# Kernel optimization log

Measured on AMD Instinct MI355X. Metric: run time of the kernel, lower is better.

## Reference

```python
import jax, jax.numpy as jnp
import numpy as np

N_RAYS = 32768
HID = 64
MARCH_ITERS = 64
EPS = 1e-4
NEAR = 0.0
FAR = 1.0
T_FAR = 1.0
TPUT_B = 64
JITTER = 1.0 / TPUT_B  # fixed stand-in for random.random() * (2 / batch_size)


def _init_linear(key, fan_in, fan_out):
    kw, kb = jax.random.split(key)
    lim = 1.0 / np.sqrt(fan_in)
    W = jax.random.uniform(kw, (fan_in, fan_out), jnp.float32, -lim, lim)
    b = jax.random.uniform(kb, (fan_out,), jnp.float32, -lim, lim)
    return W, b


def setup_inputs() -> dict:
    key = jax.random.key(0)
    ks = jax.random.split(key, 6)
    rays = jax.random.normal(ks[0], (N_RAYS, 6), jnp.float32)
    W0, b0 = _init_linear(ks[1], 3, HID)
    W1, b1 = _init_linear(ks[2], HID, HID)
    W2, b2 = _init_linear(ks[3], HID, 1)
    Wr0, br0 = _init_linear(ks[4], 6, HID)
    Wr1, br1 = _init_linear(ks[5], HID, 3)
    return dict(rays=rays, W0=W0, b0=b0, W1=W1, b1=b1, W2=W2, b2=b2,
                Wr0=Wr0, br0=br0, Wr1=Wr1, br1=br1)


def _sdf(p, W0, b0, W1, b1, W2, b2):
    # p: [N, 3] -> signed distance [N, 1]
    h = jax.nn.relu(p @ W0 + b0)
    h = jax.nn.relu(h @ W1 + b1)
    return h @ W2 + b2


def _refl(p, d, Wr0, br0, Wr1, br1):
    # p, d: [N, 3] -> RGB [N, 3]
    h = jax.nn.relu(jnp.concatenate([p, d], axis=-1) @ Wr0 + br0)
    return jax.nn.sigmoid(h @ Wr1 + br1)


def reference(rays, W0, b0, W1, b1, W2, b2, Wr0, br0, Wr1, br1):
    r_o, r_d = rays[..., :3], rays[..., 3:]
    sdf = lambda p: _sdf(p, W0, b0, W1, b1, W2, b2)

    # --- sphere march (64 fixed iterations; early-exit break is a no-op
    # once all rays hit, since hit rays stop updating) ---
    hits0 = jnp.zeros(r_o.shape[:-1] + (1,), jnp.bool_)
    dist0 = jnp.full(r_o.shape[:-1] + (1,), NEAR, jnp.float32)

    def march(carry, _):
        hits, cd = carry
        d = sdf(r_o + r_d * cd)  # [N, 1]
        hits = hits | ((d < EPS) & (cd >= NEAR) & (cd <= FAR))
        cd = jnp.where(~hits, cd + d, cd)
        return (hits, cd), None

    (hit, t), _ = jax.lax.scan(march, (hits0, dist0), None, length=MARCH_ITERS)
    pts = r_o + r_d * t

    rgb = _refl(pts, r_d, Wr0, br0, Wr1, br1)
    rgb = jnp.where(hit, rgb, 0.0)  # out[~hit] = 0

    # --- throughput (index search under no_grad in the original) ---
    max_t = T_FAR + JITTER
    step = max_t / TPUT_B
    sg = jax.lax.stop_gradient
    sdf_ng = lambda p: _sdf(p, sg(W0), sg(b0), sg(W1), sg(b1), sg(W2), sg(b2))
    r_o_ng, r_d_ng = sg(r_o), sg(r_d)

    curr_min0 = sdf_ng(r_o_ng)[..., 0]          # [N]
    idxs0 = jnp.zeros_like(curr_min0, jnp.int32)

    def tloop(carry, i):
        cm, idxs = carry
        t_i = step * (i + 1).astype(jnp.float32)
        sd = sdf_ng(r_o_ng + t_i * r_d_ng)[..., 0]
        idxs = jnp.where(sd < cm, i + 1, idxs)
        return (jnp.minimum(cm, sd), idxs), None

    (_, idxs), _ = jax.lax.scan(tloop, (curr_min0, idxs0),
                                jnp.arange(TPUT_B, dtype=jnp.int32))

    best_pos = r_o + idxs[..., None].astype(jnp.float32) * step * r_d  # [N, 3]
    tput = sdf(best_pos)  # [N, 1], differentiable (outside no_grad in torch)

    return jnp.concatenate([rgb, tput], axis=-1)  # [N, 4]
```

## Files before the change

kernel.cpp:

```cpp
#include <hip/hip_runtime.h>
#include <math.h>

#define NRAYS        32768
#define MARCH_ITERS  64
#define EPS_         1e-4f
#define STEP_        ((1.0f + 1.0f/64.0f) / 64.0f)

typedef __attribute__((ext_vector_type(8)))  short    short8;
typedef __attribute__((ext_vector_type(4)))  float    float4v;
typedef __attribute__((ext_vector_type(2)))  float    float2v;
typedef __attribute__((ext_vector_type(4)))  unsigned uint4v;

__device__ __forceinline__ short8 mk_frag(unsigned p0, unsigned p1,
                                          unsigned p2, unsigned p3) {
    uint4v v = {p0, p1, p2, p3};
    return __builtin_bit_cast(short8, v);
}

__device__ __forceinline__ unsigned packbf(unsigned a, unsigned b) {
    return __builtin_amdgcn_perm(b, a, 0x07060302u);
}

struct Split2 { unsigned h, r; };
__device__ __forceinline__ Split2 split2(float x) {
    unsigned xu = __float_as_uint(x);
    float xh = __uint_as_float(xu & 0xFFFF0000u);
    float rr = x - xh;
    return { xu, __float_as_uint(rr) };
}

__device__ __forceinline__ float2v fma2(float2v a, float2v b, float2v c) {
    return __builtin_elementwise_fma(a, b, c);
}

__global__ __launch_bounds__(64)
__attribute__((amdgpu_waves_per_eu(2, 8)))
void sdf_w11_k(
    const float* __restrict__ rays,
    const float* __restrict__ W0,  const float* __restrict__ b0,
    const float* __restrict__ W1,  const float* __restrict__ b1,
    const float* __restrict__ W2,  const float* __restrict__ b2,
    const float* __restrict__ Wr0, const float* __restrict__ br0,
    const float* __restrict__ Wr1, const float* __restrict__ br1,
    float* __restrict__ out)
{
    const int lane = threadIdx.x;
    const int quad = lane >> 4;
    const int m    = lane & 15;
    const int rayBase = blockIdx.x * 16;

    const float* rp = rays + (rayBase + m) * 6;
    const float ox = rp[0], oy = rp[1], oz = rp[2];
    const float dx = rp[3], dy = rp[4], dz = rp[5];

    float2v a2[4][2], s2[4][2];
    #pragma unroll
    for (int t = 0; t < 4; ++t)
        #pragma unroll
        for (int p = 0; p < 2; ++p) {
            float av[2], sv[2];
            #pragma unroll
            for (int e = 0; e < 2; ++e) {
                int j = 32 * (t >> 1) + 8 * quad + 4 * (t & 1) + (2 * p + e);
                float w0c = W0[j], w1c = W0[64 + j], w2c = W0[128 + j];
                av[e] = fmaf(ox, w0c, fmaf(oy, w1c, fmaf(oz, w2c, b0[j])));
                sv[e] = fmaf(dx, w0c, fmaf(dy, w1c, dz * w2c));
            }
            a2[t][p] = (float2v){av[0], av[1]};
            s2[t][p] = (float2v){sv[0], sv[1]};
        }

    float4v b1v[4];
    float2v w2a[4], w2b[4];
    #pragma unroll
    for (int t = 0; t < 4; ++t) {
        int base = 16 * t + 4 * quad;
        b1v[t] = (float4v){b1[base], b1[base + 1], b1[base + 2], b1[base + 3]};
        w2a[t] = (float2v){W2[base], W2[base + 1]};
        w2b[t] = (float2v){W2[base + 2], W2[base + 3]};
    }
    const float b2s = b2[0];

    short8 A2h[2][4], A2m[2][4];
    #pragma unroll
    for (int h = 0; h < 2; ++h)
        #pragma unroll
        for (int t = 0; t < 4; ++t) {
            unsigned pm[4], ph[4];
            #pragma unroll
            for (int jp = 0; jp < 4; ++jp) {
                int k0 = 32 * h + quad * 8 + 2 * jp;
                int j2 = 16 * t + m;
                Split2 a = split2(W1[k0 * 64 + j2]);
                Split2 b = split2(W1[(k0 + 1) * 64 + j2]);
                pm[jp] = packbf(a.r, b.r);
                ph[jp] = packbf(a.h, b.h);
            }
            A2m[h][t] = mk_frag(pm[0], pm[1], pm[2], pm[3]);
            A2h[h][t] = mk_frag(ph[0], ph[1], ph[2], ph[3]);
        }

    auto front = [&](float cv, short8* BH, short8* BM) {
        const float2v c2 = {cv, cv};
        unsigned PH[4][2], PM[4][2];
        #pragma unroll
        for (int t = 0; t < 4; ++t) {
            float2v v01 = fma2(c2, s2[t][0], a2[t][0]);
            float2v v23 = fma2(c2, s2[t][1], a2[t][1]);
            float v0 = fmaxf(v01.x, 0.f), v1 = fmaxf(v01.y, 0.f);
            float v2 = fmaxf(v23.x, 0.f), v3 = fmaxf(v23.y, 0.f);
            unsigned u0 = __float_as_uint(v0), u1 = __float_as_uint(v1);
            unsigned u2 = __float_as_uint(v2), u3 = __float_as_uint(v3);
            PH[t][0] = packbf(u0, u1); PH[t][1] = packbf(u2, u3);
            float2v h01 = {__uint_as_float(u0 & 0xFFFF0000u),
                           __uint_as_float(u1 & 0xFFFF0000u)};
            float2v h23 = {__uint_as_float(u2 & 0xFFFF0000u),
                           __uint_as_float(u3 & 0xFFFF0000u)};
            float2v r01 = (float2v){v0, v1} - h01;
            float2v r23 = (float2v){v2, v3} - h23;
            PM[t][0] = packbf(__float_as_uint(r01.x), __float_as_uint(r01.y));
            PM[t][1] = packbf(__float_as_uint(r23.x), __float_as_uint(r23.y));
        }
        #pragma unroll
        for (int h = 0; h < 2; ++h) {
            BH[h] = mk_frag(PH[2 * h][0], PH[2 * h][1],
                            PH[2 * h + 1][0], PH[2 * h + 1][1]);
            BM[h] = mk_frag(PM[2 * h][0], PM[2 * h][1],
                            PM[2 * h + 1][0], PM[2 * h + 1][1]);
        }
    };

    auto l3 = [&](const float4v* C2) -> float {
        float2v q01 = {0.f, 0.f}, q23 = {0.f, 0.f};
        #pragma unroll
        for (int t = 0; t < 4; ++t) {
            float2v rel01 = {fmaxf(C2[t][0], 0.f), fmaxf(C2[t][1], 0.f)};
            float2v rel23 = {fmaxf(C2[t][2], 0.f), fmaxf(C2[t][3], 0.f)};
            q01 = fma2(rel01, w2a[t], q01);
            q23 = fma2(rel23, w2b[t], q23);
        }
        float part = (q01.x + q01.y) + (q23.x + q23.y);
        part += __shfl_xor(part, 16, 64);
        part += __shfl_xor(part, 32, 64);
        return b2s + part;
    };

    auto tputC2 = [&](const short8* BHt, const short8* BMt, float4v* C2t) {
        #pragma unroll
        for (int t = 0; t < 4; ++t)
            C2t[t] = __builtin_amdgcn_mfma_f32_16x16x32_bf16(
                A2h[0][t], BMt[0], b1v[t], 0, 0, 0);
        #pragma unroll
        for (int t = 0; t < 4; ++t)
            C2t[t] = __builtin_amdgcn_mfma_f32_16x16x32_bf16(
                A2h[1][t], BMt[1], C2t[t], 0, 0, 0);
        #pragma unroll
        for (int h = 0; h < 2; ++h)
            #pragma unroll
            for (int t = 0; t < 4; ++t)
                C2t[t] = __builtin_amdgcn_mfma_f32_16x16x32_bf16(
                    A2h[h][t], BHt[h], C2t[t], 0, 0, 0);
    };

    bool  hit = false;
    float cd  = 0.f;
    float cm  = 3.4e38f;
    int   i   = 0;

    #pragma unroll 1
    for (; i <= 64; ++i) {
        if (i >= MARCH_ITERS || __all(hit)) break;
        float ti = STEP_ * (float)i;
        short8 BHt[2], BMt[2];
        front(ti, BHt, BMt);
        short8 BHm[2], BMm[2];
        front(cd, BHm, BMm);
        float4v C2m[4], C2t[4];
        #pragma unroll
        for (int t = 0; t < 4; ++t)
            C2m[t] = __builtin_amdgcn_mfma_f32_16x16x32_bf16(
                A2m[0][t], BHm[0], b1v[t], 0, 0, 0);
        #pragma unroll
        for (int t = 0; t < 4; ++t)
            C2m[t] = __builtin_amdgcn_mfma_f32_16x16x32_bf16(
                A2m[1][t], BHm[1], C2m[t], 0, 0, 0);
        #pragma unroll
        for (int h = 0; h < 2; ++h)
            #pragma unroll
            for (int t = 0; t < 4; ++t)
                C2m[t] = __builtin_amdgcn_mfma_f32_16x16x32_bf16(
                    A2h[h][t], BMm[h], C2m[t], 0, 0, 0);
        #pragma unroll
        for (int h = 0; h < 2; ++h)
            #pragma unroll
            for (int t = 0; t < 4; ++t)
                C2m[t] = __builtin_amdgcn_mfma_f32_16x16x32_bf16(
                    A2h[h][t], BHm[h], C2m[t], 0, 0, 0);
        tputC2(BHt, BMt, C2t);
        float dm = l3(C2m);
        bool c = (dm < EPS_) && (cd >= 0.f) && (cd <= 1.f);
        hit = hit || c;
        if (!hit) cd += dm;
        cm = fminf(cm, l3(C2t));
    }

    #pragma unroll 1
    for (; i <= 64; ++i) {
        float ti = STEP_ * (float)i;
        short8 BHt[2], BMt[2];
        front(ti, BHt, BMt);
        float4v C2t[4];
        tputC2(BHt, BMt, C2t);
        cm = fminf(cm, l3(C2t));
    }

    const float px = fmaf(dx, cd, ox), py = fmaf(dy, cd, oy), pz = fmaf(dz, cd, oz);
    float r0 = 0.f, r1 = 0.f, r2 = 0.f;
    #pragma unroll 4
    for (int jj = 0; jj < 16; ++jj) {
        int j = quad * 16 + jj;
        float a = fmaf(px, Wr0[j],
                  fmaf(py, Wr0[64 + j],
                  fmaf(pz, Wr0[128 + j],
                  fmaf(dx, Wr0[192 + j],
                  fmaf(dy, Wr0[256 + j],
                  fmaf(dz, Wr0[320 + j], br0[j]))))));
        a = fmaxf(a, 0.f);
        r0 = fmaf(a, Wr1[j * 3 + 0], r0);
        r1 = fmaf(a, Wr1[j * 3 + 1], r1);
        r2 = fmaf(a, Wr1[j * 3 + 2], r2);
    }
    r0 += __shfl_xor(r0, 16, 64); r0 += __shfl_xor(r0, 32, 64);
    r1 += __shfl_xor(r1, 16, 64); r1 += __shfl_xor(r1, 32, 64);
    r2 += __shfl_xor(r2, 16, 64); r2 += __shfl_xor(r2, 32, 64);
    r0 = 1.f / (1.f + expf(-(r0 + br1[0])));
    r1 = 1.f / (1.f + expf(-(r1 + br1[1])));
    r2 = 1.f / (1.f + expf(-(r2 + br1[2])));
    if (!hit) { r0 = 0.f; r1 = 0.f; r2 = 0.f; }
    if (lane < 16) {
        float4v o4 = {r0, r1, r2, cm};
        *reinterpret_cast<float4v*>(out + (rayBase + lane) * 4) = o4;
    }
}

extern "C" void kernel_launch(void* const* d_in, const int* in_sizes, int n_in,
                              void* d_out, int out_size, void* d_ws, size_t ws_size,
                              hipStream_t stream) {
    const float* rays = (const float*)d_in[0];
    const float* W0   = (const float*)d_in[1];
    const float* b0   = (const float*)d_in[2];
    const float* W1   = (const float*)d_in[3];
    const float* b1   = (const float*)d_in[4];
    const float* W2   = (const float*)d_in[5];
    const float* b2   = (const float*)d_in[6];
    const float* Wr0  = (const float*)d_in[7];
    const float* br0  = (const float*)d_in[8];
    const float* Wr1  = (const float*)d_in[9];
    const float* br1  = (const float*)d_in[10];
    float* out = (float*)d_out;

    hipLaunchKernelGGL(sdf_w11_k, dim3(NRAYS / 16), dim3(64), 0, stream,
                       rays, W0, b0, W1, b1, W2, b2, Wr0, br0, Wr1, br1, out);
}
```

Before: 167.9 us.

## Software-pipeline throughput front-end and use ds_swizzle for xor-16 reductions

Restructures the march loop so the throughput sample's bf16 front-end fragments for step i+1 are computed while step i's MFMAs run, issuing the throughput MFMA chain first. It also uses packed float2 max for the ReLUs, replaces the xor-16 shuffle with a ds_swizzle, and pins waves_per_eu to 2. The aim is to hide VALU front-end latency behind matrix ops and cut cross-lane cost. The cost is extra live fragment registers, and the fixed occupancy hint may limit latency hiding.

```diff
diff --git a/kernel.cpp b/kernel.cpp
--- a/kernel.cpp
+++ b/kernel.cpp
@@ -33,9 +33,18 @@
     return __builtin_elementwise_fma(a, b, c);
 }
 
+__device__ __forceinline__ float xor16_sum(float x) {
+    float p = __int_as_float(
+        __builtin_amdgcn_ds_swizzle(__float_as_int(x), 0x401F));
+    return x + p;
+}
+__device__ __forceinline__ float xor32_sum(float x) {
+    return x + __shfl_xor(x, 32, 64);
+}
+
 __global__ __launch_bounds__(64)
-__attribute__((amdgpu_waves_per_eu(2, 8)))
-void sdf_w11_k(
+__attribute__((amdgpu_waves_per_eu(2, 2)))
+void sdf_w13_k(
     const float* __restrict__ rays,
     const float* __restrict__ W0,  const float* __restrict__ b0,
     const float* __restrict__ W1,  const float* __restrict__ b1,
@@ -100,6 +109,7 @@
             A2h[h][t] = mk_frag(ph[0], ph[1], ph[2], ph[3]);
         }
 
+    const float2v z2 = {0.f, 0.f};
     auto front = [&](float cv, short8* BH, short8* BM) {
         const float2v c2 = {cv, cv};
         unsigned PH[4][2], PM[4][2];
@@ -107,17 +117,17 @@
         for (int t = 0; t < 4; ++t) {
             float2v v01 = fma2(c2, s2[t][0], a2[t][0]);
             float2v v23 = fma2(c2, s2[t][1], a2[t][1]);
-            float v0 = fmaxf(v01.x, 0.f), v1 = fmaxf(v01.y, 0.f);
-            float v2 = fmaxf(v23.x, 0.f), v3 = fmaxf(v23.y, 0.f);
-            unsigned u0 = __float_as_uint(v0), u1 = __float_as_uint(v1);
-            unsigned u2 = __float_as_uint(v2), u3 = __float_as_uint(v3);
+            v01 = __builtin_elementwise_max(v01, z2);
+            v23 = __builtin_elementwise_max(v23, z2);
+            unsigned u0 = __float_as_uint(v01.x), u1 = __float_as_uint(v01.y);
+            unsigned u2 = __float_as_uint(v23.x), u3 = __float_as_uint(v23.y);
             PH[t][0] = packbf(u0, u1); PH[t][1] = packbf(u2, u3);
             float2v h01 = {__uint_as_float(u0 & 0xFFFF0000u),
                            __uint_as_float(u1 & 0xFFFF0000u)};
             float2v h23 = {__uint_as_float(u2 & 0xFFFF0000u),
                            __uint_as_float(u3 & 0xFFFF0000u)};
-            float2v r01 = (float2v){v0, v1} - h01;
-            float2v r23 = (float2v){v2, v3} - h23;
+            float2v r01 = v01 - h01;
+            float2v r23 = v23 - h23;
             PM[t][0] = packbf(__float_as_uint(r01.x), __float_as_uint(r01.y));
             PM[t][1] = packbf(__float_as_uint(r23.x), __float_as_uint(r23.y));
         }
@@ -134,14 +144,16 @@
         float2v q01 = {0.f, 0.f}, q23 = {0.f, 0.f};
         #pragma unroll
         for (int t = 0; t < 4; ++t) {
-            float2v rel01 = {fmaxf(C2[t][0], 0.f), fmaxf(C2[t][1], 0.f)};
-            float2v rel23 = {fmaxf(C2[t][2], 0.f), fmaxf(C2[t][3], 0.f)};
+            float2v rel01 = __builtin_elementwise_max(
+                (float2v){C2[t][0], C2[t][1]}, z2);
+            float2v rel23 = __builtin_elementwise_max(
+                (float2v){C2[t][2], C2[t][3]}, z2);
             q01 = fma2(rel01, w2a[t], q01);
             q23 = fma2(rel23, w2b[t], q23);
         }
         float part = (q01.x + q01.y) + (q23.x + q23.y);
-        part += __shfl_xor(part, 16, 64);
-        part += __shfl_xor(part, 32, 64);
+        part = xor16_sum(part);
+        part = xor32_sum(part);
         return b2s + part;
     };
 
@@ -167,15 +179,19 @@
     float cm  = 3.4e38f;
     int   i   = 0;
 
+    short8 BHt[2], BMt[2];
+    front(0.f, BHt, BMt);
+
     #pragma unroll 1
-    for (; i <= 64; ++i) {
-        if (i >= MARCH_ITERS || __all(hit)) break;
-        float ti = STEP_ * (float)i;
-        short8 BHt[2], BMt[2];
-        front(ti, BHt, BMt);
+    for (; i < MARCH_ITERS; ++i) {
+        if (__all(hit)) break;
+        float4v C2t[4];
+        tputC2(BHt, BMt, C2t);
+        short8 BHtN[2], BMtN[2];
+        front(STEP_ * (float)(i + 1), BHtN, BMtN);
         short8 BHm[2], BMm[2];
         front(cd, BHm, BMm);
-        float4v C2m[4], C2t[4];
+        float4v C2m[4];
         #pragma unroll
         for (int t = 0; t < 4; ++t)
             C2m[t] = __builtin_amdgcn_mfma_f32_16x16x32_bf16(
@@ -196,22 +212,22 @@
             for (int t = 0; t < 4; ++t)
                 C2m[t] = __builtin_amdgcn_mfma_f32_16x16x32_bf16(
                     A2h[h][t], BHm[h], C2m[t], 0, 0, 0);
-        tputC2(BHt, BMt, C2t);
         float dm = l3(C2m);
         bool c = (dm < EPS_) && (cd >= 0.f) && (cd <= 1.f);
         hit = hit || c;
         if (!hit) cd += dm;
         cm = fminf(cm, l3(C2t));
+        BHt[0] = BHtN[0]; BHt[1] = BHtN[1];
+        BMt[0] = BMtN[0]; BMt[1] = BMtN[1];
     }
 
     #pragma unroll 1
     for (; i <= 64; ++i) {
-        float ti = STEP_ * (float)i;
-        short8 BHt[2], BMt[2];
-        front(ti, BHt, BMt);
         float4v C2t[4];
         tputC2(BHt, BMt, C2t);
         cm = fminf(cm, l3(C2t));
+        if (i < 64)
+            front(STEP_ * (float)(i + 1), BHt, BMt);
     }
 
     const float px = fmaf(dx, cd, ox), py = fmaf(dy, cd, oy), pz = fmaf(dz, cd, oz);
@@ -230,9 +246,9 @@
         r1 = fmaf(a, Wr1[j * 3 + 1], r1);
         r2 = fmaf(a, Wr1[j * 3 + 2], r2);
     }
-    r0 += __shfl_xor(r0, 16, 64); r0 += __shfl_xor(r0, 32, 64);
-    r1 += __shfl_xor(r1, 16, 64); r1 += __shfl_xor(r1, 32, 64);
-    r2 += __shfl_xor(r2, 16, 64); r2 += __shfl_xor(r2, 32, 64);
+    r0 = xor16_sum(r0); r0 = xor32_sum(r0);
+    r1 = xor16_sum(r1); r1 = xor32_sum(r1);
+    r2 = xor16_sum(r2); r2 = xor32_sum(r2);
     r0 = 1.f / (1.f + expf(-(r0 + br1[0])));
     r1 = 1.f / (1.f + expf(-(r1 + br1[1])));
     r2 = 1.f / (1.f + expf(-(r2 + br1[2])));
@@ -259,6 +275,6 @@
     const float* br1  = (const float*)d_in[10];
     float* out = (float*)d_out;
 
-    hipLaunchKernelGGL(sdf_w11_k, dim3(NRAYS / 16), dim3(64), 0, stream,
+    hipLaunchKernelGGL(sdf_w13_k, dim3(NRAYS / 16), dim3(64), 0, stream,
                        rays, W0, b0, W1, b1, W2, b2, Wr0, br0, Wr1, br1, out);
 }
```

Measured after the change: 171.8 us. +2.4%, slower.
